# Optimization experiments

Hardware: AMD Instinct MI355X
Metric: run time of the kernel (lower is better)

## Reference

```python
import jax, jax.numpy as jnp
import numpy as np

EPS = 1e-5
NEG_SLOPE = 0.2
NUM_ITER = 3
C = 32            # channel
LCAPS = 40        # latent_caps_size
LVEC = 40         # latent_vec_size
PCAPS = 1287      # prim_caps_size (937 + 234 + 116)


def conv1d(x, w, stride, pad):
    # x: [B, Cin, L], w: [Cout, Cin, K]
    return jax.lax.conv_general_dilated(
        x, w, window_strides=(stride,), padding=[(pad, pad)],
        dimension_numbers=('NCH', 'OIH', 'NCH'))


def bn_lrelu(x, g, b, m, v):
    # eval-mode BatchNorm1d + LeakyReLU(0.2); x: [B, C, L]
    scale = (g * jax.lax.rsqrt(v + EPS))[None, :, None]
    y = (x - m[None, :, None]) * scale + b[None, :, None]
    return jnp.where(y >= 0, y, NEG_SLOPE * y)


def squash(t):
    sn = jnp.sum(t * t, axis=-1, keepdims=True)
    return sn * t / ((1.0 + sn) * jnp.sqrt(sn))


def setup_inputs() -> dict:
    key = jax.random.key(0)
    ks = jax.random.split(key, 10)
    data = jax.random.normal(ks[0], (32, 1, 4681), jnp.float32)
    conv1_w = 0.1 * jax.random.normal(ks[1], (C, 1, 5), jnp.float32)
    conv2_w = 0.1 * jax.random.normal(ks[2], (C, C, 5), jnp.float32)
    conv3_w = 0.1 * jax.random.normal(ks[3], (C, C, 4), jnp.float32)
    lin_w = 0.1 * jax.random.normal(ks[4], (C, C, 1), jnp.float32)
    bn_gamma = 1.0 + 0.1 * jax.random.normal(ks[5], (4, C), jnp.float32)
    bn_beta = 0.1 * jax.random.normal(ks[6], (4, C), jnp.float32)
    bn_mean = 0.1 * jax.random.normal(ks[7], (4, C), jnp.float32)
    bn_var = 0.5 + jax.random.uniform(ks[8], (4, C), jnp.float32)
    W_caps = 0.01 * jax.random.normal(ks[9], (LCAPS, PCAPS, LVEC, C), jnp.float32)
    return dict(data=data, conv1_w=conv1_w, conv2_w=conv2_w, conv3_w=conv3_w,
                lin_w=lin_w, bn_gamma=bn_gamma, bn_beta=bn_beta,
                bn_mean=bn_mean, bn_var=bn_var, W_caps=W_caps)


def reference(data, conv1_w, conv2_w, conv3_w, lin_w,
              bn_gamma, bn_beta, bn_mean, bn_var, W_caps):
    # OctreeKeyConv (eval mode: BN uses running stats, dropout off)
    x1 = bn_lrelu(conv1d(data, conv1_w, 5, 2), bn_gamma[0], bn_beta[0], bn_mean[0], bn_var[0])  # [B,32,937]
    x2 = bn_lrelu(conv1d(x1, conv2_w, 4, 0), bn_gamma[1], bn_beta[1], bn_mean[1], bn_var[1])    # [B,32,234]
    x3 = bn_lrelu(conv1d(x2, conv3_w, 2, 0), bn_gamma[2], bn_beta[2], bn_mean[2], bn_var[2])    # [B,32,116]
    x = jnp.concatenate([x1, x2, x3], axis=2)                                                    # [B,32,1287]
    x = bn_lrelu(conv1d(x, lin_w, 1, 0), bn_gamma[3], bn_beta[3], bn_mean[3], bn_var[3])
    x = jnp.transpose(x, (0, 2, 1))  # [B, 1287, 32]

    # LatentCapsLayer: u_hat[b,l,p,v] = sum_s W[l,p,v,s] x[b,p,s]
    u_hat = jnp.einsum('lpvs,bps->blpv', W_caps, x)  # [B,40,1287,40]
    u_det = jax.lax.stop_gradient(u_hat)
    B = x.shape[0]
    b_ij = jnp.zeros((B, LCAPS, PCAPS), x.dtype)
    v = None
    for it in range(NUM_ITER):
        c = jax.nn.softmax(b_ij, axis=1)  # softmax over latent caps
        if it == NUM_ITER - 1:
            v = squash(jnp.sum(c[..., None] * u_hat, axis=2, keepdims=True))  # [B,40,1,40]
        else:
            v = squash(jnp.sum(c[..., None] * u_det, axis=2, keepdims=True))
            b_ij = b_ij + jnp.sum(v * u_det, axis=-1)
    latent = jnp.squeeze(v, axis=2)       # [B,40,40]
    return jnp.sum(latent, axis=-1)       # [B,40]
```

## Files before the change

### kernel.cpp

```cpp
#include <hip/hip_runtime.h>

#define EPSB 1e-5f
#define NEG 0.2f

__device__ __forceinline__ float lrelu(float y) { return y >= 0.f ? y : NEG * y; }

typedef const __attribute__((address_space(1))) unsigned int gas1_u32;
typedef __attribute__((address_space(3))) unsigned int as3_u32;
__device__ __forceinline__ void gload16nt(const float* g, float* l) {
  __builtin_amdgcn_global_load_lds((gas1_u32*)g, (as3_u32*)l, 16, 0, 2);
}
#define WAITVM(N) asm volatile("s_waitcnt vmcnt(" #N ")" ::: "memory")

typedef float floatx4 __attribute__((ext_vector_type(4)));
typedef short bf16x8 __attribute__((ext_vector_type(8)));
__device__ __forceinline__ void nt_store4(float4 v, float* addr) {
  floatx4 w = {v.x, v.y, v.z, v.w};
  __builtin_nontemporal_store(w, (floatx4*)addr);
}

__device__ __forceinline__ void barrier_nodrain() {
  asm volatile("s_waitcnt lgkmcnt(0)" ::: "memory");
  __builtin_amdgcn_s_barrier();
  __builtin_amdgcn_sched_barrier(0);
}

__global__ __launch_bounds__(256) void k_front(
    const float* __restrict__ data, const float* __restrict__ w1,
    const float* __restrict__ w2, const float* __restrict__ w3,
    const float* __restrict__ lw, const float* __restrict__ bg,
    const float* __restrict__ bb, const float* __restrict__ bm,
    const float* __restrict__ bv, float* __restrict__ xt)
{
  __shared__ float x1s[32][132];
  __shared__ float x2s[32][40];
  __shared__ float x3s[32][20];
  const int b = blockIdx.x >> 3, q = blockIdx.x & 7, t = threadIdx.x;
  const int o1s = (937*q)/8, o1e = (937*(q+1))/8;
  const int o2s = (234*q)/8, o2e = (234*(q+1))/8;
  const int o3s = (116*q)/8, o3e = (116*(q+1))/8;
  int n2s = min(o2s, 2*o3s);
  int n2e = max(o2e, 2*(o3e-1)+4); if (n2e > 234) n2e = 234;
  int n1s = min(o1s, 4*n2s);
  int n1e = max(o1e, 4*(n2e-1)+5); if (n1e > 937) n1e = 937;
  const int w1w = n1e - n1s, w2w = n2e - n2s, w3w = o3e - o3s;

  for (int idx = t; idx < 32*w1w; idx += 256) {
    int c = idx / w1w, j = n1s + idx % w1w;
    float acc = 0.f;
    int base = 5*j - 2;
    #pragma unroll
    for (int k = 0; k < 5; ++k) {
      int pos = base + k;
      float d = (pos >= 0 && pos < 4681) ? data[b*4681 + pos] : 0.f;
      acc += w1[c*5 + k] * d;
    }
    float sc = bg[c] * rsqrtf(bv[c] + EPSB);
    x1s[c][j - n1s] = lrelu((acc - bm[c]) * sc + bb[c]);
  }
  __syncthreads();
  for (int idx = t; idx < 32*w2w; idx += 256) {
    int c = idx / w2w, j = n2s + idx % w2w;
    float acc = 0.f;
    int col = 4*j - n1s;
    for (int ci = 0; ci < 32; ++ci) {
      #pragma unroll
      for (int k = 0; k < 5; ++k) acc += w2[(c*32 + ci)*5 + k] * x1s[ci][col + k];
    }
    float sc = bg[32+c] * rsqrtf(bv[32+c] + EPSB);
    x2s[c][j - n2s] = lrelu((acc - bm[32+c]) * sc + bb[32+c]);
  }
  __syncthreads();
  for (int idx = t; idx < 32*w3w; idx += 256) {
    int c = idx / w3w, j = o3s + idx % w3w;
    float acc = 0.f;
    int col = 2*j - n2s;
    for (int ci = 0; ci < 32; ++ci) {
      #pragma unroll
      for (int k = 0; k < 4; ++k) acc += w3[(c*32 + ci)*4 + k] * x2s[ci][col + k];
    }
    float sc = bg[64+c] * rsqrtf(bv[64+c] + EPSB);
    x3s[c][j - o3s] = lrelu((acc - bm[64+c]) * sc + bb[64+c]);
  }
  __syncthreads();
  const int np1 = o1e - o1s, np2 = o2e - o2s, np3 = o3e - o3s;
  const int np = np1 + np2 + np3;
  for (int idx = t; idx < np*32; idx += 256) {
    int pi = idx >> 5, s = idx & 31;
    float acc = 0.f;
    int p;
    if (pi < np1) {
      int j = o1s + pi; p = j;
      int col = j - n1s;
      for (int ci = 0; ci < 32; ++ci) acc += lw[s*32 + ci] * x1s[ci][col];
    } else if (pi < np1 + np2) {
      int j = o2s + (pi - np1); p = 937 + j;
      int col = j - n2s;
      for (int ci = 0; ci < 32; ++ci) acc += lw[s*32 + ci] * x2s[ci][col];
    } else {
      int j = o3s + (pi - np1 - np2); p = 1171 + j;
      int col = j - o3s;
      for (int ci = 0; ci < 32; ++ci) acc += lw[s*32 + ci] * x3s[ci][col];
    }
    float sc = bg[96+s] * rsqrtf(bv[96+s] + EPSB);
    xt[p*1024 + b*32 + s] = lrelu((acc - bm[96+s]) * sc + bb[96+s]);
  }
}

__global__ __launch_bounds__(256) void k_uhat(
    const float* __restrict__ W, const float* __restrict__ xt,
    float* __restrict__ u, float* __restrict__ s0part)
{
  extern __shared__ float lds[];
  float* wbuf = lds;
  unsigned short* xs_hi = (unsigned short*)(lds + 10240);
  unsigned short* xs_lo = xs_hi + 10240;
  const int t = threadIdx.x;
  const int wv = t >> 6, lane = t & 63;
  const int wi = blockIdx.x*4 + wv;
  const int l = wi % 40, chunk = wi / 40;
  const int p0 = chunk * 8;
  float* myw = wbuf + wv * 2560;
  const float* Wl = W + (size_t)l * 1287 * 1280;
  const int row = lane & 15, g = lane >> 4;

  for (int idx = t; idx < 2048; idx += 256) {
    int pl = idx >> 8, rem = idx & 255;
    int b = rem >> 3, s4 = rem & 7;
    int pg = p0 + pl;
    float4 v = make_float4(0.f, 0.f, 0.f, 0.f);
    if (pg < 1287) v = *(const float4*)(xt + pg*1024 + b*32 + s4*4);
    unsigned int b0 = __float_as_uint(v.x), b1 = __float_as_uint(v.y);
    unsigned int b2 = __float_as_uint(v.z), b3 = __float_as_uint(v.w);
    ushort4 h, lo;
    h.x = (unsigned short)(b0 >> 16); h.y = (unsigned short)(b1 >> 16);
    h.z = (unsigned short)(b2 >> 16); h.w = (unsigned short)(b3 >> 16);
    lo.x = (unsigned short)(__float_as_uint(v.x - __uint_as_float(b0 & 0xffff0000u)) >> 16);
    lo.y = (unsigned short)(__float_as_uint(v.y - __uint_as_float(b1 & 0xffff0000u)) >> 16);
    lo.z = (unsigned short)(__float_as_uint(v.z - __uint_as_float(b2 & 0xffff0000u)) >> 16);
    lo.w = (unsigned short)(__float_as_uint(v.w - __uint_as_float(b3 & 0xffff0000u)) >> 16);
    int off = pl*1280 + b*40 + s4*4;
    *(ushort4*)(xs_hi + off) = h;
    *(ushort4*)(xs_lo + off) = lo;
  }
  #pragma unroll
  for (int i = 0; i < 5; ++i) {
    int gg = i*64 + lane, v = gg >> 3, s4 = (gg & 7) ^ (v & 7);
    gload16nt(Wl + (size_t)p0*1280 + (v*8 + s4)*4, myw + i*256);
  }
  #pragma unroll
  for (int i = 0; i < 5; ++i) {
    int gg = i*64 + lane, v = gg >> 3, s4 = (gg & 7) ^ (v & 7);
    gload16nt(Wl + (size_t)(p0+1)*1280 + (v*8 + s4)*4, myw + 1280 + i*256);
  }
  __syncthreads();

  floatx4 s0acc[2][3];
  #pragma unroll
  for (int mt = 0; mt < 2; ++mt)
    #pragma unroll
    for (int nt = 0; nt < 3; ++nt)
      s0acc[mt][nt] = (floatx4){0.f, 0.f, 0.f, 0.f};

  #pragma unroll
  for (int pp = 0; pp < 8; ++pp) {
    const int p = p0 + pp;
    if (p >= 1287) break;
    if (pp == 1)      WAITVM(11);
    else if (pp >= 2 && pp <= 6) WAITVM(17);
    else if (pp == 7) WAITVM(12);
    const float* wb = myw + (pp & 1)*1280;
    const unsigned short* xh = xs_hi + pp*1280;
    const unsigned short* xl = xs_lo + pp*1280;
    bf16x8 aH[2], aL[2];
    aH[0] = *(const bf16x8*)(xh + row*40 + g*8);
    aH[1] = *(const bf16x8*)(xh + (16 + row)*40 + g*8);
    aL[0] = *(const bf16x8*)(xl + row*40 + g*8);
    aL[1] = *(const bf16x8*)(xl + (16 + row)*40 + g*8);
    floatx4 acc[2][3];
    #pragma unroll
    for (int mt = 0; mt < 2; ++mt)
      #pragma unroll
      for (int nt = 0; nt < 3; ++nt)
        acc[mt][nt] = (floatx4){0.f, 0.f, 0.f, 0.f};
    #pragma unroll
    for (int nt = 0; nt < 3; ++nt) {
      int vq = nt*16 + row;
      bool valid = vq < 40;
      int vv = valid ? vq : 0;
      float4 w0 = *(const float4*)(wb + vv*32 + (((2*g) ^ (vv & 7)) << 2));
      float4 w1 = *(const float4*)(wb + vv*32 + (((2*g + 1) ^ (vv & 7)) << 2));
      float ws[8] = {w0.x, w0.y, w0.z, w0.w, w1.x, w1.y, w1.z, w1.w};
      bf16x8 bH, bL;
      #pragma unroll
      for (int j = 0; j < 8; ++j) {
        unsigned int bits = __float_as_uint(ws[j]);
        unsigned short hs = (unsigned short)(bits >> 16);
        float lf = ws[j] - __uint_as_float(bits & 0xffff0000u);
        unsigned short lsv = (unsigned short)(__float_as_uint(lf) >> 16);
        bH[j] = valid ? (short)hs : (short)0;
        bL[j] = valid ? (short)lsv : (short)0;
      }
      #pragma unroll
      for (int mt = 0; mt < 2; ++mt) {
        acc[mt][nt] = __builtin_amdgcn_mfma_f32_16x16x32_bf16(aH[mt], bH, acc[mt][nt], 0, 0, 0);
        acc[mt][nt] = __builtin_amdgcn_mfma_f32_16x16x32_bf16(aH[mt], bL, acc[mt][nt], 0, 0, 0);
        acc[mt][nt] = __builtin_amdgcn_mfma_f32_16x16x32_bf16(aL[mt], bH, acc[mt][nt], 0, 0, 0);
      }
    }
    if (pp < 6) {
      int psrc = p + 2; if (psrc > 1286) psrc = 1286;
      asm volatile("s_waitcnt lgkmcnt(0)" ::: "memory");
      __builtin_amdgcn_sched_barrier(0);
      #pragma unroll
      for (int i = 0; i < 5; ++i) {
        int gg = i*64 + lane, v = gg >> 3, s4 = (gg & 7) ^ (v & 7);
        gload16nt(Wl + (size_t)psrc*1280 + (v*8 + s4)*4, myw + (pp & 1)*1280 + i*256);
      }
    }
    #pragma unroll
    for (int mt = 0; mt < 2; ++mt)
      #pragma unroll
      for (int nt = 0; nt < 3; ++nt) {
        int vq = nt*16 + row;
        if (vq < 40) {
          int q4 = mt*4 + g;
          *(floatx4*)(u + ((size_t)(q4*1287 + p))*6400 + l*160 + vq*4) = acc[mt][nt];
          s0acc[mt][nt] += acc[mt][nt];
        }
      }
  }
  #pragma unroll
  for (int mt = 0; mt < 2; ++mt)
    #pragma unroll
    for (int nt = 0; nt < 3; ++nt) {
      int vq = nt*16 + row;
      if (vq < 40) {
        int q4 = mt*4 + g;
        *(floatx4*)(s0part + (size_t)chunk*51200 + l*1280 + vq*32 + q4*4) = s0acc[mt][nt];
      }
    }
}

__global__ __launch_bounds__(64) void k_squash0(
    const float* __restrict__ s0, float* __restrict__ v0t)
{
  const int b = blockIdx.x / 40, l = blockIdx.x % 40, t = threadIdx.x;
  float s = 0.f;
  if (t < 40) s = s0[(l*40 + t)*32 + b] * (1.f/40.f);
  float sq = s*s;
  #pragma unroll
  for (int d = 1; d < 64; d <<= 1) sq += __shfl_xor(sq, d);
  float scale = sq > 0.f ? sq / ((1.f + sq) * sqrtf(sq)) : 0.f;
  if (t < 40) v0t[((size_t)(b >> 2)*1600 + l*40 + t)*4 + (b & 3)] = s * scale;
}

__global__ __launch_bounds__(64) void k_squash1(
    const float* __restrict__ sred, float* __restrict__ v1t)
{
  const int b = blockIdx.x / 40, l = blockIdx.x % 40, t = threadIdx.x;
  float s = 0.f;
  size_t off = ((size_t)(b >> 2)*1600 + l*40 + t)*4 + (b & 3);
  if (t < 40) s = sred[off];
  float sq = s*s;
  #pragma unroll
  for (int d = 1; d < 64; d <<= 1) sq += __shfl_xor(sq, d);
  float scale = sq > 0.f ? sq / ((1.f + sq) * sqrtf(sq)) : 0.f;
  if (t < 40) v1t[off] = s * scale;
}

__global__ __launch_bounds__(64) void k_final(
    const float* __restrict__ sred, float* __restrict__ out)
{
  const int b = blockIdx.x / 40, l = blockIdx.x % 40, t = threadIdx.x;
  float s = 0.f;
  if (t < 40) s = sred[((size_t)(b >> 2)*1600 + l*40 + t)*4 + (b & 3)];
  float sq = s*s, ss = s;
  #pragma unroll
  for (int d = 1; d < 64; d <<= 1) { sq += __shfl_xor(sq, d); ss += __shfl_xor(ss, d); }
  float scale = sq > 0.f ? sq / ((1.f + sq) * sqrtf(sq)) : 0.f;
  if (t == 0) out[b*40 + l] = ss * scale;
}

#define RPC 13
#define NCHUNK 99
__global__ __launch_bounds__(400) void k_route5(
    const float* __restrict__ u, const float* __restrict__ vprev,
    float* __restrict__ b1g, float* __restrict__ spart, int pass)
{
  __shared__ float4 dred[400];
  __shared__ float dot_lds[160];
  __shared__ float c_lds[160];
  const int q4 = blockIdx.x & 7;
  const int chunk0 = blockIdx.x >> 3;
  const int chunk = (pass == 1) ? (NCHUNK - 1 - chunk0) : chunk0;
  const int t = threadIdx.x;
  const int l = t / 10;
  const int p0 = chunk * RPC;
  const float4* u4 = (const float4*)u;
  const float4* vp4 = (const float4*)vprev + (size_t)q4*1600;

  float4 vv[4], s4[4], uu[3][4];
  float bprev[3] = {0.f, 0.f, 0.f};
  #pragma unroll
  for (int j = 0; j < 4; ++j) {
    vv[j] = vp4[t*4 + j];
    s4[j] = make_float4(0.f, 0.f, 0.f, 0.f);
  }
  {
    const float4* up0 = u4 + ((size_t)q4*1287 + p0)*1600;
    const float4* up1 = u4 + ((size_t)q4*1287 + p0 + 1)*1600;
    #pragma unroll
    for (int j = 0; j < 4; ++j) { uu[0][j] = up0[t*4 + j]; uu[1][j] = up1[t*4 + j]; }
    if (pass == 2 && t < 160) {
      bprev[0] = b1g[((size_t)q4*1287 + p0)*160 + t];
      bprev[1] = b1g[((size_t)q4*1287 + p0 + 1)*160 + t];
    }
  }

  #pragma unroll
  for (int pl = 0; pl < RPC; ++pl) {
    const int cur = pl % 3, pf = (pl + 2) % 3;
    const size_t qp = (size_t)q4*1287 + p0 + pl;
    float4 dp = make_float4(0.f, 0.f, 0.f, 0.f);
    #pragma unroll
    for (int j = 0; j < 4; ++j) {
      dp.x += uu[cur][j].x*vv[j].x; dp.y += uu[cur][j].y*vv[j].y;
      dp.z += uu[cur][j].z*vv[j].z; dp.w += uu[cur][j].w*vv[j].w;
    }
    dred[t] = dp;
    if (pl + 2 < RPC) {
      const float4* upn = u4 + (qp + 2)*1600;
      #pragma unroll
      for (int j = 0; j < 4; ++j) uu[pf][j] = upn[t*4 + j];
      if (pass == 2 && t < 160) bprev[pf] = b1g[(qp + 2)*160 + t];
    }
    barrier_nodrain();
    if (t < 160) {
      const int lr = t >> 2, b4 = t & 3;
      float d = 0.f;
      #pragma unroll
      for (int vq = 0; vq < 10; ++vq)
        d += ((const float*)&dred[lr*10 + vq])[b4];
      if (pass == 2) d += bprev[cur];
      else           b1g[qp*160 + t] = d;
      dot_lds[b4*40 + lr] = d;
    }
    barrier_nodrain();
    if (t < 256) {
      const int b4 = t >> 6, ll = t & 63;
      float d = (ll < 40) ? dot_lds[b4*40 + ll] : -1e30f;
      float m = d;
      #pragma unroll
      for (int off = 32; off; off >>= 1) m = fmaxf(m, __shfl_xor(m, off));
      float e = expf(d - m);
      float Z = e;
      #pragma unroll
      for (int off = 32; off; off >>= 1) Z += __shfl_xor(Z, off);
      if (ll < 40) c_lds[b4*40 + ll] = e * (1.f / Z);
    }
    barrier_nodrain();
    {
      float c0 = c_lds[l], c1 = c_lds[40 + l], c2 = c_lds[80 + l], c3 = c_lds[120 + l];
      #pragma unroll
      for (int j = 0; j < 4; ++j) {
        s4[j].x += uu[cur][j].x*c0; s4[j].y += uu[cur][j].y*c1;
        s4[j].z += uu[cur][j].z*c2; s4[j].w += uu[cur][j].w*c3;
      }
    }
  }
  float* sp = spart + ((size_t)chunk*8 + q4)*6400;
  #pragma unroll
  for (int j = 0; j < 4; ++j)
    nt_store4(s4[j], sp + (t*4 + j)*4);
}

__global__ __launch_bounds__(256) void k_reduceN(
    const float* __restrict__ src, float* __restrict__ sout, int n)
{
  const int w = blockIdx.x*256 + threadIdx.x;
  float s = 0.f;
  #pragma unroll 4
  for (int c = 0; c < n; ++c)
    s += __builtin_nontemporal_load(src + (size_t)c*51200 + w);
  sout[w] = s;
}

extern "C" void kernel_launch(void* const* d_in, const int* in_sizes, int n_in,
                              void* d_out, int out_size, void* d_ws, size_t ws_size,
                              hipStream_t stream)
{
  const float* data = (const float*)d_in[0];
  const float* w1   = (const float*)d_in[1];
  const float* w2   = (const float*)d_in[2];
  const float* w3   = (const float*)d_in[3];
  const float* lw   = (const float*)d_in[4];
  const float* bg   = (const float*)d_in[5];
  const float* bb   = (const float*)d_in[6];
  const float* bm   = (const float*)d_in[7];
  const float* bv   = (const float*)d_in[8];
  const float* W    = (const float*)d_in[9];
  float* out = (float*)d_out;

  float* u      = (float*)d_ws;
  float* s0     = u + 65894400;
  float* v0t    = s0 + 51200;
  float* v1t    = v0t + 51200;
  float* s1     = v1t + 51200;
  float* xt     = s1 + 51200;
  float* big    = xt + 1317888;
  float* s0part = big;
  float* b1g    = big;
  float* spart  = b1g + 1647360;

  const int KU_LDS = 10240*4 + 2*10240*2;
  hipFuncSetAttribute((const void*)k_uhat,
                      hipFuncAttributeMaxDynamicSharedMemorySize, KU_LDS);

  k_front<<<256, 256, 0, stream>>>(data, w1, w2, w3, lw, bg, bb, bm, bv, xt);
  k_uhat<<<1610, 256, KU_LDS, stream>>>(W, xt, u, s0part);
  k_reduceN<<<200, 256, 0, stream>>>(s0part, s0, 161);
  k_squash0<<<1280, 64, 0, stream>>>(s0, v0t);

  k_route5<<<NCHUNK*8, 400, 0, stream>>>(u, v0t, b1g, spart, 1);
  k_reduceN<<<200, 256, 0, stream>>>(spart, s1, NCHUNK);
  k_squash1<<<1280, 64, 0, stream>>>(s1, v1t);

  k_route5<<<NCHUNK*8, 400, 0, stream>>>(u, v1t, b1g, spart, 2);
  k_reduceN<<<200, 256, 0, stream>>>(spart, s0, NCHUNK);
  k_final<<<1280, 64, 0, stream>>>(s0, out);
}
```

Measured before the change: 376.6 us.

## Coalesce u loads in routing kernel and reduce dot products via padded LDS

The routing kernel now has each thread load float4 elements strided by 400 instead of four consecutive float4s, so neighbouring lanes touch neighbouring addresses in global memory. Each thread no longer reduces its partial dot product locally. It writes the individual products into a padded transposed LDS array, and 160 threads each sum 40 entries. The aim is better global-load coalescing, paid for with four times more LDS writes and longer serial LDS reductions inside each row iteration. For the whole thing to stay consistent, the layout of v, u and the partial sums must agree with the new lane-to-element mapping.

Result: slower. 630.7 us (+67.5%).

```diff
diff --git a/kernel.cpp b/kernel.cpp
--- a/kernel.cpp
+++ b/kernel.cpp
@@ -284,18 +284,18 @@
 
 #define RPC 13
 #define NCHUNK 99
-__global__ __launch_bounds__(400) void k_route5(
+__global__ __launch_bounds__(400) void k_route6(
     const float* __restrict__ u, const float* __restrict__ vprev,
     float* __restrict__ b1g, float* __restrict__ spart, int pass)
 {
-  __shared__ float4 dred[400];
+  __shared__ float dred_t[4*40*41];
   __shared__ float dot_lds[160];
   __shared__ float c_lds[160];
   const int q4 = blockIdx.x & 7;
   const int chunk0 = blockIdx.x >> 3;
   const int chunk = (pass == 1) ? (NCHUNK - 1 - chunk0) : chunk0;
   const int t = threadIdx.x;
-  const int l = t / 10;
+  const int l0 = t / 40, myvq = t % 40;
   const int p0 = chunk * RPC;
   const float4* u4 = (const float4*)u;
   const float4* vp4 = (const float4*)vprev + (size_t)q4*1600;
@@ -304,14 +304,14 @@
   float bprev[3] = {0.f, 0.f, 0.f};
   #pragma unroll
   for (int j = 0; j < 4; ++j) {
-    vv[j] = vp4[t*4 + j];
+    vv[j] = vp4[j*400 + t];
     s4[j] = make_float4(0.f, 0.f, 0.f, 0.f);
   }
   {
     const float4* up0 = u4 + ((size_t)q4*1287 + p0)*1600;
     const float4* up1 = u4 + ((size_t)q4*1287 + p0 + 1)*1600;
     #pragma unroll
-    for (int j = 0; j < 4; ++j) { uu[0][j] = up0[t*4 + j]; uu[1][j] = up1[t*4 + j]; }
+    for (int j = 0; j < 4; ++j) { uu[0][j] = up0[j*400 + t]; uu[1][j] = up1[j*400 + t]; }
     if (pass == 2 && t < 160) {
       bprev[0] = b1g[((size_t)q4*1287 + p0)*160 + t];
       bprev[1] = b1g[((size_t)q4*1287 + p0 + 1)*160 + t];
@@ -322,17 +322,18 @@
   for (int pl = 0; pl < RPC; ++pl) {
     const int cur = pl % 3, pf = (pl + 2) % 3;
     const size_t qp = (size_t)q4*1287 + p0 + pl;
-    float4 dp = make_float4(0.f, 0.f, 0.f, 0.f);
     #pragma unroll
     for (int j = 0; j < 4; ++j) {
-      dp.x += uu[cur][j].x*vv[j].x; dp.y += uu[cur][j].y*vv[j].y;
-      dp.z += uu[cur][j].z*vv[j].z; dp.w += uu[cur][j].w*vv[j].w;
-    }
-    dred[t] = dp;
+      const int lj = j*10 + l0;
+      dred_t[(0*40 + lj)*41 + myvq] = uu[cur][j].x * vv[j].x;
+      dred_t[(1*40 + lj)*41 + myvq] = uu[cur][j].y * vv[j].y;
+      dred_t[(2*40 + lj)*41 + myvq] = uu[cur][j].z * vv[j].z;
+      dred_t[(3*40 + lj)*41 + myvq] = uu[cur][j].w * vv[j].w;
+    }
     if (pl + 2 < RPC) {
       const float4* upn = u4 + (qp + 2)*1600;
       #pragma unroll
-      for (int j = 0; j < 4; ++j) uu[pf][j] = upn[t*4 + j];
+      for (int j = 0; j < 4; ++j) uu[pf][j] = upn[j*400 + t];
       if (pass == 2 && t < 160) bprev[pf] = b1g[(qp + 2)*160 + t];
     }
     barrier_nodrain();
@@ -340,8 +341,7 @@
       const int lr = t >> 2, b4 = t & 3;
       float d = 0.f;
       #pragma unroll
-      for (int vq = 0; vq < 10; ++vq)
-        d += ((const float*)&dred[lr*10 + vq])[b4];
+      for (int vq = 0; vq < 40; ++vq) d += dred_t[(b4*40 + lr)*41 + vq];
       if (pass == 2) d += bprev[cur];
       else           b1g[qp*160 + t] = d;
       dot_lds[b4*40 + lr] = d;
@@ -360,19 +360,19 @@
       if (ll < 40) c_lds[b4*40 + ll] = e * (1.f / Z);
     }
     barrier_nodrain();
-    {
-      float c0 = c_lds[l], c1 = c_lds[40 + l], c2 = c_lds[80 + l], c3 = c_lds[120 + l];
-      #pragma unroll
-      for (int j = 0; j < 4; ++j) {
-        s4[j].x += uu[cur][j].x*c0; s4[j].y += uu[cur][j].y*c1;
-        s4[j].z += uu[cur][j].z*c2; s4[j].w += uu[cur][j].w*c3;
-      }
+    #pragma unroll
+    for (int j = 0; j < 4; ++j) {
+      const int lj = j*10 + l0;
+      s4[j].x += uu[cur][j].x * c_lds[lj];
+      s4[j].y += uu[cur][j].y * c_lds[40 + lj];
+      s4[j].z += uu[cur][j].z * c_lds[80 + lj];
+      s4[j].w += uu[cur][j].w * c_lds[120 + lj];
     }
   }
   float* sp = spart + ((size_t)chunk*8 + q4)*6400;
   #pragma unroll
   for (int j = 0; j < 4; ++j)
-    nt_store4(s4[j], sp + (t*4 + j)*4);
+    nt_store4(s4[j], sp + (j*400 + t)*4);
 }
 
 __global__ __launch_bounds__(256) void k_reduceN(
@@ -422,11 +422,11 @@
   k_reduceN<<<200, 256, 0, stream>>>(s0part, s0, 161);
   k_squash0<<<1280, 64, 0, stream>>>(s0, v0t);
 
-  k_route5<<<NCHUNK*8, 400, 0, stream>>>(u, v0t, b1g, spart, 1);
+  k_route6<<<NCHUNK*8, 400, 0, stream>>>(u, v0t, b1g, spart, 1);
   k_reduceN<<<200, 256, 0, stream>>>(spart, s1, NCHUNK);
   k_squash1<<<1280, 64, 0, stream>>>(s1, v1t);
 
-  k_route5<<<NCHUNK*8, 400, 0, stream>>>(u, v1t, b1g, spart, 2);
+  k_route6<<<NCHUNK*8, 400, 0, stream>>>(u, v1t, b1g, spart, 2);
   k_reduceN<<<200, 256, 0, stream>>>(spart, s0, NCHUNK);
   k_final<<<1280, 64, 0, stream>>>(s0, out);
 }
```
